# Performance work log

Hardware: AMD Instinct MI355X
Metric: run time of the kernel (lower is better)

Reference implementation:

```python
import jax, jax.numpy as jnp
import numpy as np

B, T, M = 8, 4096, 1024
EPS = 1e-6
WINDOW = 15.0
INIT_GATE_BIAS = -3.0


def setup_inputs() -> dict:
    key = jax.random.key(0)
    k1, _ = jax.random.split(key)
    x = jax.random.normal(k1, (B, T, M), dtype=jnp.float32)
    # causal mask as in typical usage: lower-triangular (T, T)
    mask = jnp.tril(jnp.ones((T, T), dtype=jnp.float32))
    # learned gate parameter initialized to init_gate_bias
    gate_raw = jnp.full((M,), INIT_GATE_BIAS, dtype=jnp.float32)
    return {"x": x, "mask": mask, "gate_raw": gate_raw}


def _bump_kernel(T_len: int) -> jnp.ndarray:
    # K[i,j] convex bump in (i-j), supported on j in [i-window, i], K[i,i]=1
    i = jnp.arange(T_len, dtype=jnp.float32)[:, None]
    j = jnp.arange(T_len, dtype=jnp.float32)[None, :]
    diff = jnp.clip(i - j, 0.0, WINDOW)
    u = jnp.minimum(diff / WINDOW, 1.0 - EPS)
    K = jnp.exp(1.0 - 1.0 / (1.0 - u * u + EPS))
    K = jnp.where(i - j > WINDOW, 0.0, K)
    return K


def reference(x, mask, gate_raw):
    Bv, Tv, Mv = x.shape
    K = _bump_kernel(Tv).astype(x.dtype)
    K = K * mask.reshape(Tv, Tv).astype(x.dtype)
    K = K / jnp.maximum(K.sum(-1, keepdims=True), EPS)
    phi = jnp.einsum('ij,bjm->bim', K, x)  # (B, T, M)
    gate = jax.nn.softplus(gate_raw).reshape(1, 1, Mv)
    return phi * gate
```

## Files before the change

### kernel.cpp

```cpp
#include <hip/hip_runtime.h>
#include <math.h>

#define B_ 8
#define T_ 4096
#define M_ 1024
#define TT 64
#define EPSF 1e-6f

__global__ __launch_bounds__(256) void bump_conv_kernel(
    const float* __restrict__ x,
    const float* __restrict__ gate_raw,
    float* __restrict__ out) {
  const int tiles = T_ / TT;
  const int tile = blockIdx.x % tiles;
  const int b    = blockIdx.x / tiles;
  const int t0   = tile * TT;
  const int m    = threadIdx.x * 4;

  float w[16];
  float S = 0.0f;
#pragma unroll
  for (int d = 0; d < 16; ++d) {
    float u = fminf((float)d * (1.0f / 15.0f), 1.0f - EPSF);
    float den = 1.0f - u * u + EPSF;
    w[d] = expf(1.0f - 1.0f / den);
    S += w[d];
  }
  const float rsS = 1.0f / fmaxf(S, EPSF);

  const float4 graw = *(const float4*)(gate_raw + m);
  float4 g;
  g.x = fmaxf(graw.x, 0.0f) + log1pf(expf(-fabsf(graw.x)));
  g.y = fmaxf(graw.y, 0.0f) + log1pf(expf(-fabsf(graw.y)));
  g.z = fmaxf(graw.z, 0.0f) + log1pf(expf(-fabsf(graw.z)));
  g.w = fmaxf(graw.w, 0.0f) + log1pf(expf(-fabsf(graw.w)));

  const float* xb = x   + (size_t)b * T_ * M_ + m;
  float*       ob = out + (size_t)b * T_ * M_ + m;

  float4 r[16];
  r[0] = make_float4(0.f, 0.f, 0.f, 0.f);
#pragma unroll
  for (int k = 1; k <= 15; ++k) {
    const int t = t0 - 16 + k;
    r[k] = (t >= 0) ? *(const float4*)(xb + (size_t)t * M_)
                    : make_float4(0.f, 0.f, 0.f, 0.f);
  }
  float4 nxt = *(const float4*)(xb + (size_t)t0 * M_);

  for (int c = 0; c < TT / 16; ++c) {
#pragma unroll
    for (int s = 0; s < 16; ++s) {
      const int t = t0 + c * 16 + s;
      const float4 cur = nxt;
      const int tn = t + 1;
      if (tn < T_) nxt = *(const float4*)(xb + (size_t)tn * M_);
      r[s] = cur;

      float ax = 0.f, ay = 0.f, az = 0.f, aw = 0.f;
#pragma unroll
      for (int d = 0; d < 16; ++d) {
        const float4 v = r[(s - d + 16) & 15];
        const float wd = w[d];
        ax = fmaf(wd, v.x, ax);
        ay = fmaf(wd, v.y, ay);
        az = fmaf(wd, v.z, az);
        aw = fmaf(wd, v.w, aw);
      }

      float sc = rsS;
      if (t < 15) {
        float p = 0.0f;
#pragma unroll
        for (int d = 0; d < 16; ++d) p += (d <= t) ? w[d] : 0.0f;
        sc = 1.0f / fmaxf(p, EPSF);
      }

      float4 o;
      o.x = ax * sc * g.x;
      o.y = ay * sc * g.y;
      o.z = az * sc * g.z;
      o.w = aw * sc * g.w;
      *(float4*)(ob + (size_t)t * M_) = o;
    }
  }
}

extern "C" void kernel_launch(void* const* d_in, const int* in_sizes, int n_in,
                              void* d_out, int out_size, void* d_ws, size_t ws_size,
                              hipStream_t stream) {
  const float* x         = (const float*)d_in[0];
  const float* gate_raw  = (const float*)d_in[2];
  float*       out       = (float*)d_out;

  dim3 grid(B_ * (T_ / TT));
  dim3 block(256);
  bump_conv_kernel<<<grid, block, 0, stream>>>(x, gate_raw, out);
}
```

Measured before the change: 267.0 us.

## Shrink time tile, swizzle workgroups across XCDs, use nontemporal stores

```diff
diff --git a/kernel.cpp b/kernel.cpp
--- a/kernel.cpp
+++ b/kernel.cpp
@@ -4,16 +4,21 @@
 #define B_ 8
 #define T_ 4096
 #define M_ 1024
-#define TT 64
+#define TT 16
 #define EPSF 1e-6f
+
+typedef float fvec4 __attribute__((ext_vector_type(4)));
 
 __global__ __launch_bounds__(256) void bump_conv_kernel(
     const float* __restrict__ x,
     const float* __restrict__ gate_raw,
     float* __restrict__ out) {
   const int tiles = T_ / TT;
-  const int tile = blockIdx.x % tiles;
-  const int b    = blockIdx.x / tiles;
+  const int nwg = B_ * tiles;
+  const int cpx = nwg / 8;
+  const int lin = (blockIdx.x % 8) * cpx + blockIdx.x / 8;
+  const int tile = lin % tiles;
+  const int b    = lin / tiles;
   const int t0   = tile * TT;
   const int m    = threadIdx.x * 4;
 
@@ -28,8 +33,8 @@
   }
   const float rsS = 1.0f / fmaxf(S, EPSF);
 
-  const float4 graw = *(const float4*)(gate_raw + m);
-  float4 g;
+  const fvec4 graw = *(const fvec4*)(gate_raw + m);
+  fvec4 g;
   g.x = fmaxf(graw.x, 0.0f) + log1pf(expf(-fabsf(graw.x)));
   g.y = fmaxf(graw.y, 0.0f) + log1pf(expf(-fabsf(graw.y)));
   g.z = fmaxf(graw.z, 0.0f) + log1pf(expf(-fabsf(graw.z)));
@@ -38,51 +43,49 @@
   const float* xb = x   + (size_t)b * T_ * M_ + m;
   float*       ob = out + (size_t)b * T_ * M_ + m;
 
-  float4 r[16];
-  r[0] = make_float4(0.f, 0.f, 0.f, 0.f);
+  fvec4 r[16];
+  r[0] = (fvec4)(0.f);
 #pragma unroll
   for (int k = 1; k <= 15; ++k) {
     const int t = t0 - 16 + k;
-    r[k] = (t >= 0) ? *(const float4*)(xb + (size_t)t * M_)
-                    : make_float4(0.f, 0.f, 0.f, 0.f);
+    r[k] = (t >= 0) ? *(const fvec4*)(xb + (size_t)t * M_)
+                    : (fvec4)(0.f);
   }
-  float4 nxt = *(const float4*)(xb + (size_t)t0 * M_);
+  fvec4 nxt = *(const fvec4*)(xb + (size_t)t0 * M_);
 
-  for (int c = 0; c < TT / 16; ++c) {
 #pragma unroll
-    for (int s = 0; s < 16; ++s) {
-      const int t = t0 + c * 16 + s;
-      const float4 cur = nxt;
-      const int tn = t + 1;
-      if (tn < T_) nxt = *(const float4*)(xb + (size_t)tn * M_);
-      r[s] = cur;
+  for (int s = 0; s < 16; ++s) {
+    const int t = t0 + s;
+    const fvec4 cur = nxt;
+    if (s < 15)
+      nxt = *(const fvec4*)(xb + (size_t)(t + 1) * M_);
+    r[s] = cur;
 
-      float ax = 0.f, ay = 0.f, az = 0.f, aw = 0.f;
+    float ax = 0.f, ay = 0.f, az = 0.f, aw = 0.f;
 #pragma unroll
-      for (int d = 0; d < 16; ++d) {
-        const float4 v = r[(s - d + 16) & 15];
-        const float wd = w[d];
-        ax = fmaf(wd, v.x, ax);
-        ay = fmaf(wd, v.y, ay);
-        az = fmaf(wd, v.z, az);
-        aw = fmaf(wd, v.w, aw);
-      }
+    for (int d = 0; d < 16; ++d) {
+      const fvec4 v = r[(s - d + 16) & 15];
+      const float wd = w[d];
+      ax = fmaf(wd, v.x, ax);
+      ay = fmaf(wd, v.y, ay);
+      az = fmaf(wd, v.z, az);
+      aw = fmaf(wd, v.w, aw);
+    }
 
-      float sc = rsS;
-      if (t < 15) {
-        float p = 0.0f;
+    float sc = rsS;
+    if (t < 15) {
+      float p = 0.0f;
 #pragma unroll
-        for (int d = 0; d < 16; ++d) p += (d <= t) ? w[d] : 0.0f;
-        sc = 1.0f / fmaxf(p, EPSF);
-      }
+      for (int d = 0; d < 16; ++d) p += (d <= t) ? w[d] : 0.0f;
+      sc = 1.0f / fmaxf(p, EPSF);
+    }
 
-      float4 o;
-      o.x = ax * sc * g.x;
-      o.y = ay * sc * g.y;
-      o.z = az * sc * g.z;
-      o.w = aw * sc * g.w;
-      *(float4*)(ob + (size_t)t * M_) = o;
-    }
+    fvec4 o;
+    o.x = ax * sc * g.x;
+    o.y = ay * sc * g.y;
+    o.z = az * sc * g.z;
+    o.w = aw * sc * g.w;
+    __builtin_nontemporal_store(o, (fvec4*)(ob + (size_t)t * M_));
   }
 }
 
```

After: 268.7 us. Within noise of the previous version (+0.6%).
